# Performance work log

Measured on AMD Instinct MI355X. Metric: run time of the kernel, lower is better.

The kernel has to match this reference:

```python
import jax, jax.numpy as jnp
import numpy as np

H = 1024      # hidden_size
L = 2         # num_layers
B = 4096      # batch_size (acts as sequential time axis)
IN = 33       # LSTM input size (17 raw + 8 ip-embed + 8 port-embed)


def setup_inputs() -> dict:
    key = jax.random.key(0)
    ks = jax.random.split(key, 16)
    s = 0.02
    return {
        "x": jax.random.normal(ks[0], (B, 17), dtype=jnp.float32),
        "ip": jax.random.randint(ks[1], (B, 8), 0, 256),
        "port": jax.random.randint(ks[2], (B, 2), 0, 70000),
        "hidden": jnp.zeros((L, 1, H), dtype=jnp.float32),
        "cell": jnp.zeros((L, 1, H), dtype=jnp.float32),
        "ip_emb": jax.random.normal(ks[3], (256, 1), dtype=jnp.float32) * s,
        "port_emb": jax.random.normal(ks[4], (70000, 4), dtype=jnp.float32) * s,
        "W_ih0": jax.random.normal(ks[5], (4 * H, IN), dtype=jnp.float32) * s,
        "W_hh0": jax.random.normal(ks[6], (4 * H, H), dtype=jnp.float32) * s,
        "b_ih0": jax.random.normal(ks[7], (4 * H,), dtype=jnp.float32) * s,
        "b_hh0": jax.random.normal(ks[8], (4 * H,), dtype=jnp.float32) * s,
        "W_ih1": jax.random.normal(ks[9], (4 * H, H), dtype=jnp.float32) * s,
        "W_hh1": jax.random.normal(ks[10], (4 * H, H), dtype=jnp.float32) * s,
        "b_ih1": jax.random.normal(ks[11], (4 * H,), dtype=jnp.float32) * s,
        "b_hh1": jax.random.normal(ks[12], (4 * H,), dtype=jnp.float32) * s,
    }


def reference(x, ip, port, hidden, cell, ip_emb, port_emb,
              W_ih0, W_hh0, b_ih0, b_hh0, W_ih1, W_hh1, b_ih1, b_hh1):
    # embedding lookups + concat -> [B, 33]
    ip_e = ip_emb[ip].reshape(B, -1)        # [B, 8]
    port_e = port_emb[port].reshape(B, -1)  # [B, 8]
    xin = jnp.concatenate((x, ip_e, port_e), axis=1)  # [B, 33]

    Wih = (W_ih0, W_ih1)
    Whh = (W_hh0, W_hh1)
    bih = (b_ih0, b_ih1)
    bhh = (b_hh0, b_hh1)

    h0 = hidden[:, 0]  # [L, H]
    c0 = cell[:, 0]    # [L, H]

    def step(carry, xt):
        h, c = carry
        inp = xt
        hs, cs = [], []
        for l in range(L):  # fixed small layer loop
            gates = Wih[l] @ inp + bih[l] + Whh[l] @ h[l] + bhh[l]  # [4H]
            i, f, g, o = jnp.split(gates, 4)  # PyTorch gate order: i,f,g,o
            i = jax.nn.sigmoid(i)
            f = jax.nn.sigmoid(f)
            g = jnp.tanh(g)
            o = jax.nn.sigmoid(o)
            c_new = f * c[l] + i * g
            h_new = o * jnp.tanh(c_new)
            hs.append(h_new)
            cs.append(c_new)
            inp = h_new
        return (jnp.stack(hs), jnp.stack(cs)), jax.nn.relu(inp)

    (hf, cf), outputs = jax.lax.scan(step, (h0, c0), xin)
    return outputs, (hf[:, None, :], cf[:, None, :])
```

## Files before the change

### kernel.cpp

```cpp
#include <hip/hip_runtime.h>
#include <hip/hip_fp16.h>
#include <math.h>

#define Hn 1024
#define Bn 4096
#define INW 33
#define OUTS (Bn * Hn)
#define TPB 512

typedef _Float16 half2v __attribute__((ext_vector_type(2)));
typedef unsigned uint4v __attribute__((ext_vector_type(4)));

__device__ __forceinline__ float sigmoidf_(float x) {
    return 1.0f / (1.0f + __expf(-x));
}
__device__ __forceinline__ float tanhf_(float x) {
    float e = __expf(-2.0f * fabsf(x));
    float r = (1.0f - e) / (1.0f + e);
    return copysignf(r, x);
}
__device__ __forceinline__ unsigned pack2(float a, float b) {
    __half2 h = __floats2half2_rn(a, b);
    return __builtin_bit_cast(unsigned, h);
}
__device__ __forceinline__ float dot2acc(unsigned w, unsigned hv, float acc) {
#if __has_builtin(__builtin_amdgcn_fdot2)
    return __builtin_amdgcn_fdot2(__builtin_bit_cast(half2v, w),
                                  __builtin_bit_cast(half2v, hv), acc, false);
#else
    __half2 wh = __builtin_bit_cast(__half2, w);
    __half2 hh = __builtin_bit_cast(__half2, hv);
    float2 wf = __half22float2(wh), hf = __half22float2(hh);
    return acc + wf.x * hf.x + wf.y * hf.y;
#endif
}

__device__ __forceinline__ void probe_spin(const unsigned long long* p, unsigned tag) {
    int rounds = 0;
    for (;;) {
        unsigned long long v;
        asm volatile("global_load_dwordx2 %0, %1, off sc0 sc1\n\t"
                     "s_waitcnt vmcnt(0)"
                     : "=v"(v) : "v"(p) : "memory");
        if ((unsigned)(v >> 32) == tag) break;
        if (++rounds > (1 << 24)) break;
        if (rounds > 4) __builtin_amdgcn_s_sleep(1);
    }
}

__device__ __forceinline__ void poll_row(const unsigned long long* rowbase, int lane,
                                         unsigned tag, uint4v& r0, uint4v& r1,
                                         uint4v& r2, uint4v& r3) {
    const char* p = (const char*)rowbase + lane * 16;
    int rounds = 0;
    for (;;) {
        asm volatile(
            "global_load_dwordx4 %0, %4, off sc0 sc1\n\t"
            "global_load_dwordx4 %1, %4, off offset:1024 sc0 sc1\n\t"
            "global_load_dwordx4 %2, %4, off offset:2048 sc0 sc1\n\t"
            "global_load_dwordx4 %3, %4, off offset:3072 sc0 sc1\n\t"
            "s_waitcnt vmcnt(0)"
            : "=v"(r0), "=v"(r1), "=v"(r2), "=v"(r3)
            : "v"(p)
            : "memory");
        bool ok = (r0.y == tag) & (r0.w == tag) & (r1.y == tag) & (r1.w == tag)
                & (r2.y == tag) & (r2.w == tag) & (r3.y == tag) & (r3.w == tag);
        if (__all(ok)) break;
        if (++rounds > (1 << 22)) break;
        if (rounds > 2) __builtin_amdgcn_s_sleep(1);
    }
}

__device__ __forceinline__ void row_to_lds(unsigned* hs2, int base, int lane,
                                           const uint4v& r0, const uint4v& r1,
                                           const uint4v& r2, const uint4v& r3) {
    hs2[base +       2 * lane]     = r0.x;  hs2[base +       2 * lane + 1] = r0.z;
    hs2[base + 128 + 2 * lane]     = r1.x;  hs2[base + 128 + 2 * lane + 1] = r1.z;
    hs2[base + 256 + 2 * lane]     = r2.x;  hs2[base + 256 + 2 * lane + 1] = r2.z;
    hs2[base + 384 + 2 * lane]     = r3.x;  hs2[base + 384 + 2 * lane + 1] = r3.z;
}

__device__ __forceinline__ void store16_coherent(void* dst, uint4v v) {
    asm volatile("global_store_dwordx4 %0, %1, off sc0 sc1"
                 :: "v"(dst), "v"(v) : "memory");
}

__global__ void prep_kernel(const float* __restrict__ x, const int* __restrict__ ip,
                            const int* __restrict__ port, const float* __restrict__ ip_emb,
                            const float* __restrict__ port_emb, float* __restrict__ xin) {
    int gid = blockIdx.x * blockDim.x + threadIdx.x;
    if (gid < Bn * INW) {
        int t = gid / INW;
        int k = gid - t * INW;
        float v;
        if (k < 17) {
            v = x[t * 17 + k];
        } else if (k < 25) {
            v = ip_emb[ip[t * 8 + (k - 17)]];
        } else {
            int kk = k - 25;
            v = port_emb[port[t * 2 + (kk >> 2)] * 4 + (kk & 3)];
        }
        xin[gid] = v;
    }
}

__global__ void __launch_bounds__(TPB, 2) lstm_kernel(
    const float* __restrict__ xin,
    const float* __restrict__ hid0, const float* __restrict__ cel0,
    const float* __restrict__ Wih0, const float* __restrict__ Whh0,
    const float* __restrict__ bih0, const float* __restrict__ bhh0,
    const float* __restrict__ Wih1, const float* __restrict__ Whh1,
    const float* __restrict__ bih1, const float* __restrict__ bhh1,
    float* __restrict__ out,
    unsigned long long* __restrict__ h0pkt,
    unsigned long long* __restrict__ h1pkt)
{
    __shared__ unsigned hs2[1024];
    __shared__ unsigned long long stg[16];
    const int tid  = threadIdx.x;
    const int lane = tid & 63;
    const int wave = tid >> 6;
    const int bx   = blockIdx.x;

    if (bx < 32) {
        const int j0 = bx * 32 + wave * 4;
        const int probe0 = (bx * 67 + 13) & 511;
        unsigned w2[4][4][8];
        float    wx[4][4];
        float    bs[4][4];
#pragma unroll
        for (int jj = 0; jj < 4; ++jj) {
#pragma unroll
            for (int g = 0; g < 4; ++g) {
                const int row = g * Hn + (j0 + jj);
                const float* wr = Whh0 + (size_t)row * Hn;
#pragma unroll
                for (int k = 0; k < 8; ++k) {
                    int c = lane + 64 * k;
                    w2[jj][g][k] = pack2(wr[2 * c], wr[2 * c + 1]);
                }
                wx[jj][g] = (lane < INW) ? Wih0[row * INW + lane] : 0.0f;
                bs[jj][g] = bih0[row] + bhh0[row];
            }
        }
        float cst[4], hcur[4];
#pragma unroll
        for (int jj = 0; jj < 4; ++jj) { cst[jj] = cel0[j0 + jj]; hcur[jj] = 0.0f; }

        for (int t = 0; t < Bn; ++t) {
            float xv = xin[t * INW + (lane < INW ? lane : 0)];
            if (wave == 0) {
                if (t == 0) {
#pragma unroll
                    for (int m = 0; m < 8; ++m) {
                        int q = lane + 64 * m;
                        hs2[q] = pack2(hid0[2 * q], hid0[2 * q + 1]);
                    }
                } else {
                    const unsigned long long* rb = h0pkt + (size_t)(t - 1) * 512;
                    probe_spin(rb + probe0, (unsigned)t);
                    uint4v r0, r1, r2, r3;
                    poll_row(rb, lane, (unsigned)t, r0, r1, r2, r3);
                    row_to_lds(hs2, 0, lane, r0, r1, r2, r3);
                }
            }
            __syncthreads();

            float acc[4][4];
#pragma unroll
            for (int jj = 0; jj < 4; ++jj)
#pragma unroll
                for (int g = 0; g < 4; ++g) acc[jj][g] = wx[jj][g] * xv;
#pragma unroll
            for (int k = 0; k < 8; ++k) {
                unsigned hv = hs2[lane + 64 * k];
#pragma unroll
                for (int jj = 0; jj < 4; ++jj)
#pragma unroll
                    for (int g = 0; g < 4; ++g)
                        acc[jj][g] = dot2acc(w2[jj][g][k], hv, acc[jj][g]);
            }
            __syncthreads();

#pragma unroll
            for (int off = 32; off >= 1; off >>= 1)
#pragma unroll
                for (int jj = 0; jj < 4; ++jj)
#pragma unroll
                    for (int g = 0; g < 4; ++g)
                        acc[jj][g] += __shfl_xor(acc[jj][g], off);

#pragma unroll
            for (int jj = 0; jj < 4; ++jj) {
                float gi = sigmoidf_(acc[jj][0] + bs[jj][0]);
                float gf = sigmoidf_(acc[jj][1] + bs[jj][1]);
                float gg = tanhf_   (acc[jj][2] + bs[jj][2]);
                float go = sigmoidf_(acc[jj][3] + bs[jj][3]);
                cst[jj] = gf * cst[jj] + gi * gg;
                hcur[jj] = go * tanhf_(cst[jj]);
            }
            if (lane == 0) {
                unsigned long long tw = ((unsigned long long)(t + 1)) << 32;
                stg[2 * wave]     = tw | pack2(hcur[0], hcur[1]);
                stg[2 * wave + 1] = tw | pack2(hcur[2], hcur[3]);
            }
            __syncthreads();
            if (wave == 0 && lane < 8) {
                uint4v v = *(const uint4v*)&stg[2 * lane];
                char* dst = (char*)(h0pkt + (size_t)t * 512) + bx * 128 + lane * 16;
                store16_coherent(dst, v);
            }
        }
        if (lane == 0) {
#pragma unroll
            for (int jj = 0; jj < 4; ++jj) {
                out[OUTS + j0 + jj] = hcur[jj];
                out[OUTS + 2 * Hn + j0 + jj] = cst[jj];
            }
        }
    } else {
        const int blk = bx - 32;
        const int j0  = blk * 16 + wave * 2;
        const int probeA = ((blk + 64) * 67 + 13) & 511;
        const int probeB = (blk * 67 + 13) & 511;
        unsigned w2[2][4][16];
        float    bs[2][4];
#pragma unroll
        for (int jj = 0; jj < 2; ++jj) {
#pragma unroll
            for (int g = 0; g < 4; ++g) {
                const int row = g * Hn + (j0 + jj);
                const float* wr1 = Wih1 + (size_t)row * Hn;
                const float* wr2 = Whh1 + (size_t)row * Hn;
#pragma unroll
                for (int k = 0; k < 8; ++k) {
                    int c = lane + 64 * k;
                    w2[jj][g][k]     = pack2(wr1[2 * c], wr1[2 * c + 1]);
                    w2[jj][g][8 + k] = pack2(wr2[2 * c], wr2[2 * c + 1]);
                }
                bs[jj][g] = bih1[row] + bhh1[row];
            }
        }
        float cst[2], hcur[2];
#pragma unroll
        for (int jj = 0; jj < 2; ++jj) { cst[jj] = cel0[Hn + j0 + jj]; hcur[jj] = 0.0f; }

        for (int t = 0; t < Bn; ++t) {
            if (wave == 0) {
                const unsigned long long* rb = h0pkt + (size_t)t * 512;
                probe_spin(rb + probeA, (unsigned)(t + 1));
                uint4v r0, r1, r2, r3;
                poll_row(rb, lane, (unsigned)(t + 1), r0, r1, r2, r3);
                row_to_lds(hs2, 0, lane, r0, r1, r2, r3);
            } else if (wave == 1) {
                if (t == 0) {
#pragma unroll
                    for (int m = 0; m < 8; ++m) {
                        int q = lane + 64 * m;
                        hs2[512 + q] = pack2(hid0[Hn + 2 * q], hid0[Hn + 2 * q + 1]);
                    }
                } else {
                    const unsigned long long* rb = h1pkt + (size_t)(t - 1) * 512;
                    probe_spin(rb + probeB, (unsigned)t);
                    uint4v r0, r1, r2, r3;
                    poll_row(rb, lane, (unsigned)t, r0, r1, r2, r3);
                    row_to_lds(hs2, 512, lane, r0, r1, r2, r3);
                }
            }
            __syncthreads();

            float acc[2][4];
#pragma unroll
            for (int jj = 0; jj < 2; ++jj)
#pragma unroll
                for (int g = 0; g < 4; ++g) acc[jj][g] = 0.0f;
#pragma unroll
            for (int k = 0; k < 16; ++k) {
                unsigned hv = hs2[lane + 64 * k];
#pragma unroll
                for (int jj = 0; jj < 2; ++jj)
#pragma unroll
                    for (int g = 0; g < 4; ++g)
                        acc[jj][g] = dot2acc(w2[jj][g][k], hv, acc[jj][g]);
            }
            __syncthreads();

#pragma unroll
            for (int off = 32; off >= 1; off >>= 1)
#pragma unroll
                for (int jj = 0; jj < 2; ++jj)
#pragma unroll
                    for (int g = 0; g < 4; ++g)
                        acc[jj][g] += __shfl_xor(acc[jj][g], off);

#pragma unroll
            for (int jj = 0; jj < 2; ++jj) {
                float gi = sigmoidf_(acc[jj][0] + bs[jj][0]);
                float gf = sigmoidf_(acc[jj][1] + bs[jj][1]);
                float gg = tanhf_   (acc[jj][2] + bs[jj][2]);
                float go = sigmoidf_(acc[jj][3] + bs[jj][3]);
                cst[jj] = gf * cst[jj] + gi * gg;
                hcur[jj] = go * tanhf_(cst[jj]);
            }
            if (lane == 0) {
                unsigned long long tw = ((unsigned long long)(t + 1)) << 32;
                stg[wave] = tw | pack2(hcur[0], hcur[1]);
                float2 o2 = make_float2(fmaxf(hcur[0], 0.0f), fmaxf(hcur[1], 0.0f));
                *(float2*)(out + (size_t)t * Hn + j0) = o2;
            }
            __syncthreads();
            if (wave == 0 && lane < 4) {
                uint4v v = *(const uint4v*)&stg[2 * lane];
                char* dst = (char*)(h1pkt + (size_t)t * 512) + blk * 64 + lane * 16;
                store16_coherent(dst, v);
            }
        }
        if (lane == 0) {
#pragma unroll
            for (int jj = 0; jj < 2; ++jj) {
                out[OUTS + Hn + j0 + jj] = hcur[jj];
                out[OUTS + 3 * Hn + j0 + jj] = cst[jj];
            }
        }
    }
}

extern "C" void kernel_launch(void* const* d_in, const int* in_sizes, int n_in,
                              void* d_out, int out_size, void* d_ws, size_t ws_size,
                              hipStream_t stream) {
    const float* x        = (const float*)d_in[0];
    const int*   ip       = (const int*)d_in[1];
    const int*   port     = (const int*)d_in[2];
    const float* hidden   = (const float*)d_in[3];
    const float* cell     = (const float*)d_in[4];
    const float* ip_emb   = (const float*)d_in[5];
    const float* port_emb = (const float*)d_in[6];
    const float* Wih0     = (const float*)d_in[7];
    const float* Whh0     = (const float*)d_in[8];
    const float* bih0     = (const float*)d_in[9];
    const float* bhh0     = (const float*)d_in[10];
    const float* Wih1     = (const float*)d_in[11];
    const float* Whh1     = (const float*)d_in[12];
    const float* bih1     = (const float*)d_in[13];
    const float* bhh1     = (const float*)d_in[14];
    float* out = (float*)d_out;

    unsigned long long* h0pkt = (unsigned long long*)d_ws;
    unsigned long long* h1pkt = h0pkt + (size_t)Bn * 512;
    float* xin = (float*)(h1pkt + (size_t)Bn * 512);

    prep_kernel<<<dim3((Bn * INW + 255) / 256), dim3(256), 0, stream>>>(
        x, ip, port, ip_emb, port_emb, xin);

    lstm_kernel<<<dim3(96), dim3(TPB), 0, stream>>>(
        xin, hidden, cell, Wih0, Whh0, bih0, bhh0, Wih1, Whh1, bih1, bhh1,
        out, h0pkt, h1pkt);
}
```

Baseline: 17.29 ms.

## Interleave layer-0 and layer-1 hidden packets into one per-step row; drop spin sleeps

Layer-0 and layer-1 hidden-state packets now sit in a single interleaved row buffer per time step, with layer 1's output for step t placed next to layer 0's output for step t+1. The layer-1 blocks pre-publish their initial hidden state so both waves read the same row each step, which should improve locality of the polled lines. The s_sleep backoff in both polling loops is removed to cut wake-up latency on the serial critical path. In exchange, busy polling without sleep adds memory traffic and contention.

```diff
diff --git a/kernel.cpp b/kernel.cpp
--- a/kernel.cpp
+++ b/kernel.cpp
@@ -7,6 +7,7 @@
 #define INW 33
 #define OUTS (Bn * Hn)
 #define TPB 512
+#define ROWP 1024
 
 typedef _Float16 half2v __attribute__((ext_vector_type(2)));
 typedef unsigned uint4v __attribute__((ext_vector_type(4)));
@@ -44,14 +45,13 @@
                      : "=v"(v) : "v"(p) : "memory");
         if ((unsigned)(v >> 32) == tag) break;
         if (++rounds > (1 << 24)) break;
-        if (rounds > 4) __builtin_amdgcn_s_sleep(1);
     }
 }
 
-__device__ __forceinline__ void poll_row(const unsigned long long* rowbase, int lane,
+__device__ __forceinline__ void poll_row(const unsigned long long* halfbase, int lane,
                                          unsigned tag, uint4v& r0, uint4v& r1,
                                          uint4v& r2, uint4v& r3) {
-    const char* p = (const char*)rowbase + lane * 16;
+    const char* p = (const char*)halfbase + lane * 16;
     int rounds = 0;
     for (;;) {
         asm volatile(
@@ -67,7 +67,6 @@
                 & (r2.y == tag) & (r2.w == tag) & (r3.y == tag) & (r3.w == tag);
         if (__all(ok)) break;
         if (++rounds > (1 << 22)) break;
-        if (rounds > 2) __builtin_amdgcn_s_sleep(1);
     }
 }
 
@@ -113,8 +112,7 @@
     const float* __restrict__ Wih1, const float* __restrict__ Whh1,
     const float* __restrict__ bih1, const float* __restrict__ bhh1,
     float* __restrict__ out,
-    unsigned long long* __restrict__ h0pkt,
-    unsigned long long* __restrict__ h1pkt)
+    unsigned long long* __restrict__ rowpkt)
 {
     __shared__ unsigned hs2[1024];
     __shared__ unsigned long long stg[16];
@@ -148,20 +146,20 @@
 #pragma unroll
         for (int jj = 0; jj < 4; ++jj) { cst[jj] = cel0[j0 + jj]; hcur[jj] = 0.0f; }
 
-        for (int t = 0; t < Bn; ++t) {
-            float xv = xin[t * INW + (lane < INW ? lane : 0)];
+        for (int s = 0; s < Bn; ++s) {
+            float xv = xin[s * INW + (lane < INW ? lane : 0)];
             if (wave == 0) {
-                if (t == 0) {
+                if (s == 0) {
 #pragma unroll
                     for (int m = 0; m < 8; ++m) {
                         int q = lane + 64 * m;
                         hs2[q] = pack2(hid0[2 * q], hid0[2 * q + 1]);
                     }
                 } else {
-                    const unsigned long long* rb = h0pkt + (size_t)(t - 1) * 512;
-                    probe_spin(rb + probe0, (unsigned)t);
+                    const unsigned long long* rb = rowpkt + (size_t)(s - 1) * ROWP;
+                    probe_spin(rb + probe0, (unsigned)s);
                     uint4v r0, r1, r2, r3;
-                    poll_row(rb, lane, (unsigned)t, r0, r1, r2, r3);
+                    poll_row(rb, lane, (unsigned)s, r0, r1, r2, r3);
                     row_to_lds(hs2, 0, lane, r0, r1, r2, r3);
                 }
             }
@@ -201,14 +199,14 @@
                 hcur[jj] = go * tanhf_(cst[jj]);
             }
             if (lane == 0) {
-                unsigned long long tw = ((unsigned long long)(t + 1)) << 32;
+                unsigned long long tw = ((unsigned long long)(s + 1)) << 32;
                 stg[2 * wave]     = tw | pack2(hcur[0], hcur[1]);
                 stg[2 * wave + 1] = tw | pack2(hcur[2], hcur[3]);
             }
             __syncthreads();
             if (wave == 0 && lane < 8) {
                 uint4v v = *(const uint4v*)&stg[2 * lane];
-                char* dst = (char*)(h0pkt + (size_t)t * 512) + bx * 128 + lane * 16;
+                char* dst = (char*)(rowpkt + (size_t)s * ROWP) + bx * 128 + lane * 16;
                 store16_coherent(dst, v);
             }
         }
@@ -223,7 +221,7 @@
         const int blk = bx - 32;
         const int j0  = blk * 16 + wave * 2;
         const int probeA = ((blk + 64) * 67 + 13) & 511;
-        const int probeB = (blk * 67 + 13) & 511;
+        const int probeB = 512 + ((blk * 67 + 13) & 511);
         unsigned w2[2][4][16];
         float    bs[2][4];
 #pragma unroll
@@ -246,27 +244,28 @@
 #pragma unroll
         for (int jj = 0; jj < 2; ++jj) { cst[jj] = cel0[Hn + j0 + jj]; hcur[jj] = 0.0f; }
 
-        for (int t = 0; t < Bn; ++t) {
+        if (lane == 0)
+            stg[wave] = (1ULL << 32) | pack2(hid0[Hn + j0], hid0[Hn + j0 + 1]);
+        __syncthreads();
+        if (wave == 0 && lane < 4) {
+            uint4v v = *(const uint4v*)&stg[2 * lane];
+            char* dst = (char*)(rowpkt + 512) + blk * 64 + lane * 16;
+            store16_coherent(dst, v);
+        }
+
+        for (int s = 1; s <= Bn; ++s) {
+            const int t = s - 1;
+            const unsigned long long* rb = rowpkt + (size_t)(s - 1) * ROWP;
             if (wave == 0) {
-                const unsigned long long* rb = h0pkt + (size_t)t * 512;
-                probe_spin(rb + probeA, (unsigned)(t + 1));
+                probe_spin(rb + probeA, (unsigned)s);
                 uint4v r0, r1, r2, r3;
-                poll_row(rb, lane, (unsigned)(t + 1), r0, r1, r2, r3);
+                poll_row(rb, lane, (unsigned)s, r0, r1, r2, r3);
                 row_to_lds(hs2, 0, lane, r0, r1, r2, r3);
             } else if (wave == 1) {
-                if (t == 0) {
-#pragma unroll
-                    for (int m = 0; m < 8; ++m) {
-                        int q = lane + 64 * m;
-                        hs2[512 + q] = pack2(hid0[Hn + 2 * q], hid0[Hn + 2 * q + 1]);
-                    }
-                } else {
-                    const unsigned long long* rb = h1pkt + (size_t)(t - 1) * 512;
-                    probe_spin(rb + probeB, (unsigned)t);
-                    uint4v r0, r1, r2, r3;
-                    poll_row(rb, lane, (unsigned)t, r0, r1, r2, r3);
-                    row_to_lds(hs2, 512, lane, r0, r1, r2, r3);
-                }
+                probe_spin(rb + probeB, (unsigned)s);
+                uint4v r0, r1, r2, r3;
+                poll_row(rb + 512, lane, (unsigned)s, r0, r1, r2, r3);
+                row_to_lds(hs2, 512, lane, r0, r1, r2, r3);
             }
             __syncthreads();
 
@@ -304,7 +303,7 @@
                 hcur[jj] = go * tanhf_(cst[jj]);
             }
             if (lane == 0) {
-                unsigned long long tw = ((unsigned long long)(t + 1)) << 32;
+                unsigned long long tw = ((unsigned long long)(s + 1)) << 32;
                 stg[wave] = tw | pack2(hcur[0], hcur[1]);
                 float2 o2 = make_float2(fmaxf(hcur[0], 0.0f), fmaxf(hcur[1], 0.0f));
                 *(float2*)(out + (size_t)t * Hn + j0) = o2;
@@ -312,7 +311,7 @@
             __syncthreads();
             if (wave == 0 && lane < 4) {
                 uint4v v = *(const uint4v*)&stg[2 * lane];
-                char* dst = (char*)(h1pkt + (size_t)t * 512) + blk * 64 + lane * 16;
+                char* dst = (char*)(rowpkt + (size_t)s * ROWP + 512) + blk * 64 + lane * 16;
                 store16_coherent(dst, v);
             }
         }
@@ -346,14 +345,13 @@
     const float* bhh1     = (const float*)d_in[14];
     float* out = (float*)d_out;
 
-    unsigned long long* h0pkt = (unsigned long long*)d_ws;
-    unsigned long long* h1pkt = h0pkt + (size_t)Bn * 512;
-    float* xin = (float*)(h1pkt + (size_t)Bn * 512);
+    unsigned long long* rowpkt = (unsigned long long*)d_ws;
+    float* xin = (float*)(rowpkt + (size_t)(Bn + 1) * ROWP);
 
     prep_kernel<<<dim3((Bn * INW + 255) / 256), dim3(256), 0, stream>>>(
         x, ip, port, ip_emb, port_emb, xin);
 
     lstm_kernel<<<dim3(96), dim3(TPB), 0, stream>>>(
         xin, hidden, cell, Wih0, Whh0, bih0, bhh0, Wih1, Whh1, bih1, bhh1,
-        out, h0pkt, h1pkt);
-}
+        out, rowpkt);
+}
```

Result: no change. 17.23 ms (-0.4%).
